# Performance work log

Hardware: AMD Instinct MI355X
Metric: run time of the kernel (lower is better)

The kernel has to match this reference:

```python
import jax, jax.numpy as jnp
import numpy as np

N = 100_000      # nodes
E = 1_600_000    # edges
IN = 128         # input_dim
HID = 64         # hidden_dim
H = 4            # num_heads
DH = HID // H    # per-head dim
L = 3            # num_layers
OUT = 64         # output_dim
SLOPE = 0.2      # DGL GATConv LeakyReLU default
EPS = 1e-5       # LayerNorm eps


def setup_inputs() -> dict:
    key = jax.random.key(0)
    ks = jax.random.split(key, 20)
    s = 0.02
    return {
        "node_features": jax.random.normal(ks[0], (N, IN), jnp.float32),
        "src": jax.random.randint(ks[1], (E,), 0, N, jnp.int32),
        "dst": jax.random.randint(ks[2], (E,), 0, N, jnp.int32),
        # input projection
        "W_in": jax.random.normal(ks[3], (IN, HID), jnp.float32) * s,
        "b_in": jnp.zeros((HID,), jnp.float32),
        # rewiring MLP: Linear(2*HID,64) -> Tanh -> Linear(64,1) -> Sigmoid
        "W_a1": jax.random.normal(ks[4], (2 * HID, 64), jnp.float32) * s,
        "b_a1": jnp.zeros((64,), jnp.float32),
        "W_a2": jax.random.normal(ks[5], (64, 1), jnp.float32) * s,
        "b_a2": jnp.zeros((1,), jnp.float32),
        # stacked GATConv params for L layers
        "W_gat": jax.random.normal(ks[6], (L, HID, H * DH), jnp.float32) * s,
        "a_l": jax.random.normal(ks[7], (L, H, DH), jnp.float32) * s,
        "a_r": jax.random.normal(ks[8], (L, H, DH), jnp.float32) * s,
        "b_gat": jnp.zeros((L, H, DH), jnp.float32),
        # LayerNorm + output projection
        "ln_g": jnp.ones((HID,), jnp.float32),
        "ln_b": jnp.zeros((HID,), jnp.float32),
        "W_out": jax.random.normal(ks[9], (HID, OUT), jnp.float32) * s,
        "b_out": jnp.zeros((OUT,), jnp.float32),
    }


def _gat_layer(h, src, dst, W, al, ar, b):
    # h: (N, HID) -> z: (N, H, DH)
    z = (h @ W).reshape(N, H, DH)
    el = jnp.sum(z * al, axis=-1)                       # (N, H)
    er = jnp.sum(z * ar, axis=-1)                       # (N, H)
    e = jax.nn.leaky_relu(el[src] + er[dst], SLOPE)     # (E, H)
    # segment softmax over incoming edges of each dst node
    m = jax.ops.segment_max(e, dst, num_segments=N)     # (N, H)
    ex = jnp.exp(e - m[dst])                            # (E, H)
    den = jax.ops.segment_sum(ex, dst, num_segments=N)  # (N, H)
    alpha = ex / den[dst]                               # (E, H)
    msg = z[src] * alpha[..., None]                     # (E, H, DH)
    out = jax.ops.segment_sum(msg, dst, num_segments=N) # (N, H, DH)
    # residual (identity since HID == H*DH) + bias, then flatten(1)
    out = out + h.reshape(N, H, DH) + b
    return out.reshape(N, H * DH)


def reference(node_features, src, dst, W_in, b_in, W_a1, b_a1, W_a2, b_a2,
              W_gat, a_l, a_r, b_gat, ln_g, ln_b, W_out, b_out):
    h = node_features @ W_in + b_in                     # (N, HID)
    # GraphRewiringModule: edge-wise gather + MLP + sigmoid score
    he = jnp.concatenate([h[src], h[dst]], axis=1)      # (E, 2*HID)
    edge_score = jax.nn.sigmoid(jnp.tanh(he @ W_a1 + b_a1) @ W_a2 + b_a2)  # (E,1); unused downstream, as in source
    for l in range(L):
        h = _gat_layer(h, src, dst, W_gat[l], a_l[l], a_r[l], b_gat[l])
    # LayerNorm
    mu = jnp.mean(h, axis=-1, keepdims=True)
    var = jnp.mean((h - mu) ** 2, axis=-1, keepdims=True)
    h = (h - mu) * jax.lax.rsqrt(var + EPS) * ln_g + ln_b
    return h @ W_out + b_out                            # (N, OUT)
```

## Files before the change

### kernel.cpp

```cpp
#include <hip/hip_runtime.h>

#define NN 100000
#define EE 1600000
#define IN_DIM 128
#define HID 64
#define NH 4
#define DH 16
#define NL 3
#define OUT_DIM 64
#define SLOPE 0.2f
#define LN_EPS 1e-5f
#define RB 4

#define BSH 9
#define BSZ 512
#define NB ((NN + BSZ - 1) / BSZ)
#define CAP 10240
#define CHUNK 4096
#define P1_BLOCKS ((EE + CHUNK - 1) / CHUNK)

using short8 = __attribute__((ext_vector_type(8))) short;
using f32x4  = __attribute__((ext_vector_type(4))) float;

__device__ __forceinline__ float bcast(float x, int lane) {
    return __int_as_float(__builtin_amdgcn_readlane(__float_as_int(x), lane));
}
__device__ __forceinline__ unsigned f2bf(float x) {
    unsigned u = __float_as_uint(x);
    u += 0x7FFFu + ((u >> 16) & 1u);
    return u >> 16;
}
__device__ __forceinline__ float bf2f(unsigned short b) {
    return __uint_as_float(((unsigned)b) << 16);
}
__device__ __forceinline__ float bflo(unsigned zp) {
    return __uint_as_float(zp << 16);
}
__device__ __forceinline__ float bfhi(unsigned zp) {
    return __uint_as_float(zp & 0xFFFF0000u);
}

__global__ void k_wpack(const float* __restrict__ W, uint4* __restrict__ Wb) {
    const int tid = blockIdx.x * 256 + threadIdx.x;
    if (tid >= 1024) return;
    const int lane = tid & 63;
    const int ntkk = tid >> 6;
    const int nt = ntkk & 3, kk = ntkk >> 2;
    const int k0 = kk * 32 + (lane >> 4) * 8;
    const int n  = nt * 16 + (lane & 15);
    unsigned dw[4];
#pragma unroll
    for (int p = 0; p < 4; ++p) {
        const unsigned lo = f2bf(W[(k0 + 2 * p) * HID + n]);
        const unsigned hi = f2bf(W[(k0 + 2 * p + 1) * HID + n]);
        dw[p] = lo | (hi << 16);
    }
    Wb[ntkk * 64 + lane] = make_uint4(dw[0], dw[1], dw[2], dw[3]);
}

__device__ float walv(const float* __restrict__ W, const float* __restrict__ al,
                      const float* __restrict__ ar, int k, int c) {
    if (c < 4) {
        float s = 0.f;
#pragma unroll
        for (int d = 0; d < 16; ++d) s += W[k * HID + c * 16 + d] * al[c * 16 + d];
        return s;
    }
    if (c < 8) {
        const int hh = c - 4;
        float s = 0.f;
#pragma unroll
        for (int d = 0; d < 16; ++d) s += W[k * HID + hh * 16 + d] * ar[hh * 16 + d];
        return s;
    }
    return 0.f;
}

__global__ void k_wpack_gat(const float* __restrict__ W_gat, const float* __restrict__ a_l,
                            const float* __restrict__ a_r, uint4* __restrict__ Wbg) {
    const int l = blockIdx.y;
    const int tid = blockIdx.x * 256 + threadIdx.x;
    if (tid >= 640) return;
    const int lane = tid & 63;
    const int f = tid >> 6;
    const int kk = f / 5, nt = f % 5;
    const float* W  = W_gat + (size_t)l * HID * HID;
    const float* al = a_l + (size_t)l * HID;
    const float* ar = a_r + (size_t)l * HID;
    const int k0 = kk * 32 + (lane >> 4) * 8;
    const int n  = lane & 15;
    unsigned dw[4];
#pragma unroll
    for (int p = 0; p < 4; ++p) {
        float b0, b1;
        if (nt < 4) {
            b0 = W[(k0 + 2 * p) * HID + nt * 16 + n];
            b1 = W[(k0 + 2 * p + 1) * HID + nt * 16 + n];
        } else {
            b0 = walv(W, al, ar, k0 + 2 * p, n);
            b1 = walv(W, al, ar, k0 + 2 * p + 1, n);
        }
        dw[p] = f2bf(b0) | (f2bf(b1) << 16);
    }
    Wbg[(size_t)l * 640 + f * 64 + lane] = make_uint4(dw[0], dw[1], dw[2], dw[3]);
}

__global__ __launch_bounds__(256)
void k_in_gemm(const float* __restrict__ X, const uint4* __restrict__ Wb,
               const float* __restrict__ b, unsigned* __restrict__ h32) {
    const int l  = threadIdx.x & 63;
    const int wv = threadIdx.x >> 6;
    const int wrow = blockIdx.x * 64 + wv * 16;
    if (wrow >= NN) return;
    const int arow = wrow + (l & 15);
    const int kb_off = (l >> 4) * 8;
    f32x4 acc[4];
#pragma unroll
    for (int nt = 0; nt < 4; ++nt) acc[nt] = (f32x4){0.f, 0.f, 0.f, 0.f};
    const float* xr = X + (size_t)arow * IN_DIM;
#pragma unroll
    for (int kk = 0; kk < 4; ++kk) {
        const int kb = kk * 32 + kb_off;
        const float4 xa = *(const float4*)(xr + kb);
        const float4 xb = *(const float4*)(xr + kb + 4);
        const unsigned d0 = f2bf(xa.x) | (f2bf(xa.y) << 16);
        const unsigned d1 = f2bf(xa.z) | (f2bf(xa.w) << 16);
        const unsigned d2 = f2bf(xb.x) | (f2bf(xb.y) << 16);
        const unsigned d3 = f2bf(xb.z) | (f2bf(xb.w) << 16);
        const uint4 au = make_uint4(d0, d1, d2, d3);
        const short8 af = __builtin_bit_cast(short8, au);
#pragma unroll
        for (int nt = 0; nt < 4; ++nt) {
            const uint4 bu = Wb[(kk * 4 + nt) * 64 + l];
            const short8 bf = __builtin_bit_cast(short8, bu);
            acc[nt] = __builtin_amdgcn_mfma_f32_16x16x32_bf16(af, bf, acc[nt], 0, 0, 0);
        }
    }
    const int grp = l >> 4, ci = l & 15;
#pragma unroll
    for (int nt = 0; nt < 4; ++nt) {
        const float bv = b[nt * 16 + ci];
#pragma unroll
        for (int r = 0; r < 4; ++r) {
            const int row = wrow + grp * 4 + r;
            const unsigned my = f2bf(acc[nt][r] + bv);
            const unsigned ot = (unsigned)__shfl_xor((int)my, 1, 64);
            if ((ci & 1) == 0)
                h32[(size_t)row * 32 + nt * 8 + (ci >> 1)] = my | (ot << 16);
        }
    }
}

__global__ __launch_bounds__(256)
void k_zgemm(const unsigned short* __restrict__ h16, const uint4* __restrict__ Wbg,
             unsigned* __restrict__ zb32, float* __restrict__ el, float* __restrict__ er) {
    const int l  = threadIdx.x & 63;
    const int wv = threadIdx.x >> 6;
    const int wrow = blockIdx.x * 64 + wv * 16;
    if (wrow >= NN) return;
    const int arow = wrow + (l & 15);
    const int kb_off = (l >> 4) * 8;
    f32x4 acc[5];
#pragma unroll
    for (int nt = 0; nt < 5; ++nt) acc[nt] = (f32x4){0.f, 0.f, 0.f, 0.f};
#pragma unroll
    for (int kk = 0; kk < 2; ++kk) {
        const int kb = kk * 32 + kb_off;
        const uint4 au = *(const uint4*)(h16 + (size_t)arow * 64 + kb);
        const short8 af = __builtin_bit_cast(short8, au);
#pragma unroll
        for (int nt = 0; nt < 5; ++nt) {
            const uint4 bu = Wbg[(kk * 5 + nt) * 64 + l];
            const short8 bf = __builtin_bit_cast(short8, bu);
            acc[nt] = __builtin_amdgcn_mfma_f32_16x16x32_bf16(af, bf, acc[nt], 0, 0, 0);
        }
    }
    const int grp = l >> 4, ci = l & 15;
#pragma unroll
    for (int nt = 0; nt < 4; ++nt) {
#pragma unroll
        for (int r = 0; r < 4; ++r) {
            const int row = wrow + grp * 4 + r;
            const unsigned my = f2bf(acc[nt][r]);
            const unsigned ot = (unsigned)__shfl_xor((int)my, 1, 64);
            if ((ci & 1) == 0)
                zb32[(size_t)row * 32 + nt * 8 + (ci >> 1)] = my | (ot << 16);
        }
    }
#pragma unroll
    for (int r = 0; r < 4; ++r) {
        const int row = wrow + grp * 4 + r;
        const float v = acc[4][r];
        if (ci < 4) el[row * NH + ci] = v;
        else if (ci < 8) er[row * NH + (ci - 4)] = v;
    }
}


__global__ void k_zero_bcnt(int* __restrict__ bcnt, int* __restrict__ esrc_pad) {
    if (threadIdx.x < NB) bcnt[threadIdx.x] = 0;
    if (threadIdx.x < 32) esrc_pad[threadIdx.x] = 0;
}

__global__ __launch_bounds__(256)
void k_bucketize(const int* __restrict__ src, const int* __restrict__ dst,
                 int* __restrict__ bcnt, int2* __restrict__ bbuf) {
    __shared__ int lh[256];
    __shared__ int lbase[256];
    __shared__ int lcnt[256];
    __shared__ int gbase[256];
    __shared__ int sc[256];
    __shared__ int2 stage[CHUNK];
    const int t = threadIdx.x;
    const int e0 = blockIdx.x * CHUNK;
    const int n = min(CHUNK, EE - e0);
    lh[t] = 0;
    __syncthreads();
    int myd[CHUNK / 256], mys[CHUNK / 256];
#pragma unroll
    for (int i = 0; i < CHUNK / 256; ++i) {
        const int o = i * 256 + t;
        if (o < n) {
            myd[i] = dst[e0 + o];
            mys[i] = src[e0 + o];
            atomicAdd(&lh[myd[i] >> BSH], 1);
        } else myd[i] = -1;
    }
    __syncthreads();
    {
        const int v = lh[t];
        lcnt[t] = v;
        sc[t] = v;
        __syncthreads();
        for (int off = 1; off < 256; off <<= 1) {
            const int x = (t >= off) ? sc[t - off] : 0;
            __syncthreads();
            sc[t] += x;
            __syncthreads();
        }
        lbase[t] = sc[t] - v;
        lh[t] = sc[t] - v;
    }
    __syncthreads();
#pragma unroll
    for (int i = 0; i < CHUNK / 256; ++i) {
        if (myd[i] >= 0) {
            const int b = myd[i] >> BSH;
            const int p = atomicAdd(&lh[b], 1);
            stage[p] = make_int2(mys[i], myd[i]);
        }
    }
    __syncthreads();
    if (t < NB && lcnt[t] > 0) gbase[t] = atomicAdd(&bcnt[t], lcnt[t]);
    __syncthreads();
    for (int i = t; i < n; i += 256) {
        const int2 en = stage[i];
        const int b = en.y >> BSH;
        const int gp = gbase[b] + (i - lbase[b]);
        if (gp < CAP) bbuf[(size_t)b * CAP + gp] = en;
    }
}

__global__ void k_bscan(const int* __restrict__ bcnt, int* __restrict__ bbase,
                        int* __restrict__ rowptr) {
    const int t = threadIdx.x;
    __shared__ int sc[256];
    const int v = (t < NB) ? bcnt[t] : 0;
    sc[t] = v;
    __syncthreads();
    for (int off = 1; off < 256; off <<= 1) {
        const int x = (t >= off) ? sc[t - off] : 0;
        __syncthreads();
        sc[t] += x;
        __syncthreads();
    }
    if (t < NB) bbase[t] = sc[t] - v;
    if (t == 0) rowptr[NN] = EE;
}

__global__ __launch_bounds__(256)
void k_localcsr(const int* __restrict__ bcnt, const int* __restrict__ bbase,
                const int2* __restrict__ bbuf, int* __restrict__ rowptr,
                int* __restrict__ esrc) {
    const int b = blockIdx.x;
    const int t = threadIdx.x;
    const int cnt = bcnt[b];
    const int base = bbase[b];
    const int n0 = b * BSZ;
    const int nn = min(BSZ, NN - n0);
    __shared__ int lh[BSZ];
    __shared__ int lsc[BSZ];
    __shared__ int sc[256];
    for (int i = t; i < BSZ; i += 256) lh[i] = 0;
    __syncthreads();
    const int2* bb = bbuf + (size_t)b * CAP;
    for (int i = t; i < cnt; i += 256) atomicAdd(&lh[bb[i].y & (BSZ - 1)], 1);
    __syncthreads();
    const int a0 = lh[2 * t], a1 = lh[2 * t + 1];
    const int ts = a0 + a1;
    sc[t] = ts;
    __syncthreads();
    for (int off = 1; off < 256; off <<= 1) {
        const int x = (t >= off) ? sc[t - off] : 0;
        __syncthreads();
        sc[t] += x;
        __syncthreads();
    }
    const int ebase = sc[t] - ts;
    lsc[2 * t] = ebase;
    lsc[2 * t + 1] = ebase + a0;
    __syncthreads();
    for (int i = t; i < BSZ; i += 256) {
        if (i < nn) rowptr[n0 + i] = base + lsc[i];
        lh[i] = lsc[i];
    }
    __syncthreads();
    for (int i = t; i < cnt; i += 256) {
        const int2 en = bb[i];
        const int p = atomicAdd(&lh[en.y & (BSZ - 1)], 1);
        esrc[base + p] = en.x;
    }
}

__global__ __launch_bounds__(256)
void k_gat_dst(const int* __restrict__ rowptr, const int* __restrict__ esrc,
               const float* __restrict__ el, const float* __restrict__ er,
               const uint4* __restrict__ zb128, const unsigned short* __restrict__ hin16,
               const float* __restrict__ bg, unsigned* __restrict__ hout32) {
    const int j  = threadIdx.x & 63;
    const int wv = threadIdx.x >> 6;
    const int d = blockIdx.x * 4 + wv;
    if (d >= NN) return;
    const int g = j >> 3;
    const int q = j & 7;
    const int hh = q >> 1;
    const int r0 = rowptr[d], r1 = rowptr[d + 1];
    const float erh = er[d * NH + hh];
    uint4 hv4 = make_uint4(0, 0, 0, 0);
    if (g == 0) hv4 = *(const uint4*)(hin16 + (size_t)d * 64 + 8 * q);
    float a0 = 0.f, a1 = 0.f, a2 = 0.f, a3 = 0.f;
    float a4 = 0.f, a5 = 0.f, a6 = 0.f, a7 = 0.f;
    float den = 0.f;
    unsigned sA = (unsigned)esrc[r0 + g];
    float avA = el[sA * NH + hh];
    uint4 zpA = zb128[sA * 8u + q];
    unsigned sB = (unsigned)esrc[r0 + 8 + g];
    for (int i = r0; i < r1; i += 8) {
        const float avB = el[sB * NH + hh];
        const uint4 zpB = zb128[sB * 8u + q];
        const unsigned sC = (unsigned)esrc[i + 16 + g];
        const float x = avA + erh;
        float w = __expf(fmaxf(x, SLOPE * x));
        w = (i + g < r1) ? w : 0.f;
        den += w;
        a0 = fmaf(w, bflo(zpA.x), a0);
        a1 = fmaf(w, bfhi(zpA.x), a1);
        a2 = fmaf(w, bflo(zpA.y), a2);
        a3 = fmaf(w, bfhi(zpA.y), a3);
        a4 = fmaf(w, bflo(zpA.z), a4);
        a5 = fmaf(w, bfhi(zpA.z), a5);
        a6 = fmaf(w, bflo(zpA.w), a6);
        a7 = fmaf(w, bfhi(zpA.w), a7);
        sA = sB; avA = avB; zpA = zpB; sB = sC;
    }
#pragma unroll
    for (int m = 8; m <= 32; m <<= 1) {
        den += __shfl_xor(den, m, 64);
        a0 += __shfl_xor(a0, m, 64);
        a1 += __shfl_xor(a1, m, 64);
        a2 += __shfl_xor(a2, m, 64);
        a3 += __shfl_xor(a3, m, 64);
        a4 += __shfl_xor(a4, m, 64);
        a5 += __shfl_xor(a5, m, 64);
        a6 += __shfl_xor(a6, m, 64);
        a7 += __shfl_xor(a7, m, 64);
    }
    if (g == 0) {
        const int c = 8 * q;
        float o0 = bflo(hv4.x) + bg[c + 0], o1 = bfhi(hv4.x) + bg[c + 1];
        float o2 = bflo(hv4.y) + bg[c + 2], o3 = bfhi(hv4.y) + bg[c + 3];
        float o4 = bflo(hv4.z) + bg[c + 4], o5 = bfhi(hv4.z) + bg[c + 5];
        float o6 = bflo(hv4.w) + bg[c + 6], o7 = bfhi(hv4.w) + bg[c + 7];
        if (r1 > r0) {
            const float rd = 1.f / den;
            o0 = fmaf(a0, rd, o0); o1 = fmaf(a1, rd, o1);
            o2 = fmaf(a2, rd, o2); o3 = fmaf(a3, rd, o3);
            o4 = fmaf(a4, rd, o4); o5 = fmaf(a5, rd, o5);
            o6 = fmaf(a6, rd, o6); o7 = fmaf(a7, rd, o7);
        }
        const uint4 ov = make_uint4(f2bf(o0) | (f2bf(o1) << 16),
                                    f2bf(o2) | (f2bf(o3) << 16),
                                    f2bf(o4) | (f2bf(o5) << 16),
                                    f2bf(o6) | (f2bf(o7) << 16));
        *(uint4*)(hout32 + (size_t)d * 32 + 4 * q) = ov;
    }
}

__global__ __launch_bounds__(256, 4)
void k_ln_out(const unsigned short* __restrict__ h16, const float* __restrict__ g,
              const float* __restrict__ be, const float* __restrict__ Wo,
              const float* __restrict__ bo, float* __restrict__ out) {
    const int j = threadIdx.x & 63;
    float Wreg[HID];
#pragma unroll
    for (int k = 0; k < HID; ++k) Wreg[k] = Wo[k * OUT_DIM + j];
    const float gj = g[j], bej = be[j], boj = bo[j];
    const int wid = (blockIdx.x * blockDim.x + threadIdx.x) >> 6;
    const int nw  = (gridDim.x * blockDim.x) >> 6;
    for (int v0 = wid * RB; v0 < NN; v0 += nw * RB) {
        float hn[RB];
#pragma unroll
        for (int r = 0; r < RB; ++r) {
            const float x = bf2f(h16[(size_t)(v0 + r) * HID + j]);
            float s = x;
#pragma unroll
            for (int m = 32; m >= 1; m >>= 1) s += __shfl_xor(s, m, 64);
            const float mu = s * (1.f / 64.f);
            const float dx = x - mu;
            float vs = dx * dx;
#pragma unroll
            for (int m = 32; m >= 1; m >>= 1) vs += __shfl_xor(vs, m, 64);
            hn[r] = dx * rsqrtf(vs * (1.f / 64.f) + LN_EPS) * gj + bej;
        }
        float acc[RB];
#pragma unroll
        for (int r = 0; r < RB; ++r) acc[r] = boj;
#pragma unroll
        for (int k = 0; k < HID; ++k) {
#pragma unroll
            for (int r = 0; r < RB; ++r)
                acc[r] = fmaf(bcast(hn[r], k), Wreg[k], acc[r]);
        }
#pragma unroll
        for (int r = 0; r < RB; ++r) out[(size_t)(v0 + r) * OUT_DIM + j] = acc[r];
    }
}

extern "C" void kernel_launch(void* const* d_in, const int* in_sizes, int n_in,
                              void* d_out, int out_size, void* d_ws, size_t ws_size,
                              hipStream_t stream) {
    const float* X     = (const float*)d_in[0];
    const int*   src   = (const int*)d_in[1];
    const int*   dst   = (const int*)d_in[2];
    const float* W_in  = (const float*)d_in[3];
    const float* b_in  = (const float*)d_in[4];
    const float* W_gat = (const float*)d_in[9];
    const float* a_l   = (const float*)d_in[10];
    const float* a_r   = (const float*)d_in[11];
    const float* b_gat = (const float*)d_in[12];
    const float* ln_g  = (const float*)d_in[13];
    const float* ln_b  = (const float*)d_in[14];
    const float* W_out = (const float*)d_in[15];
    const float* b_out = (const float*)d_in[16];
    float* out = (float*)d_out;

    char* ws = (char*)d_ws;
    unsigned short* hA16 = (unsigned short*)ws;
    unsigned short* hB16 = hA16 + (size_t)NN * HID;
    unsigned* zb32 = (unsigned*)(hB16 + (size_t)NN * HID);
    float* el = (float*)(zb32 + (size_t)NN * (HID / 2));
    float* er = el + (size_t)NN * NH;
    int* rowptr = (int*)(er + (size_t)NN * NH);
    int* esrc   = rowptr + NN + 1;
    int* bcnt   = esrc + EE + 32;
    int* bbase  = bcnt + NB;
    uintptr_t wp = (uintptr_t)(bbase + NB);
    wp = (wp + 15) & ~(uintptr_t)15;
    uint4* Wb   = (uint4*)wp;
    uint4* Wbg  = Wb + 1024;
    int2* bbuf  = (int2*)hB16;

    k_wpack<<<4, 256, 0, stream>>>(W_in, Wb);
    k_wpack_gat<<<dim3(3, NL), 256, 0, stream>>>(W_gat, a_l, a_r, Wbg);
    k_in_gemm<<<(NN + 63) / 64, 256, 0, stream>>>(X, Wb, b_in, (unsigned*)hA16);

    k_zero_bcnt<<<1, 256, 0, stream>>>(bcnt, esrc + EE);
    k_bucketize<<<P1_BLOCKS, 256, 0, stream>>>(src, dst, bcnt, bbuf);
    k_bscan<<<1, 256, 0, stream>>>(bcnt, bbase, rowptr);
    k_localcsr<<<NB, 256, 0, stream>>>(bcnt, bbase, bbuf, rowptr, esrc);

    unsigned short* hin = hA16;
    unsigned short* hout = hB16;
    for (int l = 0; l < NL; ++l) {
        k_zgemm<<<(NN + 63) / 64, 256, 0, stream>>>(hin, Wbg + (size_t)l * 640,
                                                    zb32, el, er);
        k_gat_dst<<<(NN + 3) / 4, 256, 0, stream>>>(rowptr, esrc, el, er,
                                                    (const uint4*)zb32, hin,
                                                    b_gat + (size_t)l * HID,
                                                    (unsigned*)hout);
        unsigned short* t = hin; hin = hout; hout = t;
    }

    k_ln_out<<<1024, 256, 0, stream>>>(hin, ln_g, ln_b, W_out, b_out, out);
}
```

Baseline: 295.8 us.

## Store GAT node features as scaled FP8 and pack bucket entries into 32 bits

```diff
diff --git a/kernel.cpp b/kernel.cpp
--- a/kernel.cpp
+++ b/kernel.cpp
@@ -11,6 +11,8 @@
 #define SLOPE 0.2f
 #define LN_EPS 1e-5f
 #define RB 4
+#define ZSC 64.0f
+#define ZISC 0.015625f
 
 #define BSH 9
 #define BSZ 512
@@ -21,6 +23,7 @@
 
 using short8 = __attribute__((ext_vector_type(8))) short;
 using f32x4  = __attribute__((ext_vector_type(4))) float;
+using f32x2  = __attribute__((ext_vector_type(2))) float;
 
 __device__ __forceinline__ float bcast(float x, int lane) {
     return __int_as_float(__builtin_amdgcn_readlane(__float_as_int(x), lane));
@@ -153,7 +156,7 @@
 
 __global__ __launch_bounds__(256)
 void k_zgemm(const unsigned short* __restrict__ h16, const uint4* __restrict__ Wbg,
-             unsigned* __restrict__ zb32, float* __restrict__ el, float* __restrict__ er) {
+             unsigned* __restrict__ zb8, float* __restrict__ el, float* __restrict__ er) {
     const int l  = threadIdx.x & 63;
     const int wv = threadIdx.x >> 6;
     const int wrow = blockIdx.x * 64 + wv * 16;
@@ -181,10 +184,13 @@
 #pragma unroll
         for (int r = 0; r < 4; ++r) {
             const int row = wrow + grp * 4 + r;
-            const unsigned my = f2bf(acc[nt][r]);
-            const unsigned ot = (unsigned)__shfl_xor((int)my, 1, 64);
-            if ((ci & 1) == 0)
-                zb32[(size_t)row * 32 + nt * 8 + (ci >> 1)] = my | (ot << 16);
+            const float v = acc[nt][r] * ZSC;
+            const float vn = __shfl_xor(v, 1, 64);
+            unsigned pk = (unsigned)__builtin_amdgcn_cvt_pk_fp8_f32(v, vn, 0, false) & 0xFFFFu;
+            const unsigned pk2 = (unsigned)__shfl_xor((int)pk, 2, 64);
+            pk |= pk2 << 16;
+            if ((ci & 3) == 0)
+                zb8[(size_t)row * 16 + nt * 4 + (ci >> 2)] = pk;
         }
     }
 #pragma unroll
@@ -204,7 +210,7 @@
 
 __global__ __launch_bounds__(256)
 void k_bucketize(const int* __restrict__ src, const int* __restrict__ dst,
-                 int* __restrict__ bcnt, int2* __restrict__ bbuf) {
+                 int* __restrict__ bcnt, unsigned* __restrict__ bbuf) {
     __shared__ int lh[256];
     __shared__ int lbase[256];
     __shared__ int lcnt[256];
@@ -257,7 +263,9 @@
         const int2 en = stage[i];
         const int b = en.y >> BSH;
         const int gp = gbase[b] + (i - lbase[b]);
-        if (gp < CAP) bbuf[(size_t)b * CAP + gp] = en;
+        if (gp < CAP)
+            bbuf[(size_t)b * CAP + gp] =
+                (unsigned)en.x | (((unsigned)en.y & 511u) << 17);
     }
 }
 
@@ -280,7 +288,7 @@
 
 __global__ __launch_bounds__(256)
 void k_localcsr(const int* __restrict__ bcnt, const int* __restrict__ bbase,
-                const int2* __restrict__ bbuf, int* __restrict__ rowptr,
+                const unsigned* __restrict__ bbuf, int* __restrict__ rowptr,
                 int* __restrict__ esrc) {
     const int b = blockIdx.x;
     const int t = threadIdx.x;
@@ -293,8 +301,8 @@
     __shared__ int sc[256];
     for (int i = t; i < BSZ; i += 256) lh[i] = 0;
     __syncthreads();
-    const int2* bb = bbuf + (size_t)b * CAP;
-    for (int i = t; i < cnt; i += 256) atomicAdd(&lh[bb[i].y & (BSZ - 1)], 1);
+    const unsigned* bb = bbuf + (size_t)b * CAP;
+    for (int i = t; i < cnt; i += 256) atomicAdd(&lh[(bb[i] >> 17) & 511u], 1);
     __syncthreads();
     const int a0 = lh[2 * t], a1 = lh[2 * t + 1];
     const int ts = a0 + a1;
@@ -316,16 +324,16 @@
     }
     __syncthreads();
     for (int i = t; i < cnt; i += 256) {
-        const int2 en = bb[i];
-        const int p = atomicAdd(&lh[en.y & (BSZ - 1)], 1);
-        esrc[base + p] = en.x;
+        const unsigned en = bb[i];
+        const int p = atomicAdd(&lh[(en >> 17) & 511u], 1);
+        esrc[base + p] = (int)(en & 0x1FFFFu);
     }
 }
 
 __global__ __launch_bounds__(256)
 void k_gat_dst(const int* __restrict__ rowptr, const int* __restrict__ esrc,
                const float* __restrict__ el, const float* __restrict__ er,
-               const uint4* __restrict__ zb128, const unsigned short* __restrict__ hin16,
+               const uint2* __restrict__ zb64, const unsigned short* __restrict__ hin16,
                const float* __restrict__ bg, unsigned* __restrict__ hout32) {
     const int j  = threadIdx.x & 63;
     const int wv = threadIdx.x >> 6;
@@ -343,24 +351,28 @@
     float den = 0.f;
     unsigned sA = (unsigned)esrc[r0 + g];
     float avA = el[sA * NH + hh];
-    uint4 zpA = zb128[sA * 8u + q];
+    uint2 zpA = zb64[sA * 8u + q];
     unsigned sB = (unsigned)esrc[r0 + 8 + g];
     for (int i = r0; i < r1; i += 8) {
         const float avB = el[sB * NH + hh];
-        const uint4 zpB = zb128[sB * 8u + q];
+        const uint2 zpB = zb64[sB * 8u + q];
         const unsigned sC = (unsigned)esrc[i + 16 + g];
         const float x = avA + erh;
         float w = __expf(fmaxf(x, SLOPE * x));
         w = (i + g < r1) ? w : 0.f;
         den += w;
-        a0 = fmaf(w, bflo(zpA.x), a0);
-        a1 = fmaf(w, bfhi(zpA.x), a1);
-        a2 = fmaf(w, bflo(zpA.y), a2);
-        a3 = fmaf(w, bfhi(zpA.y), a3);
-        a4 = fmaf(w, bflo(zpA.z), a4);
-        a5 = fmaf(w, bfhi(zpA.z), a5);
-        a6 = fmaf(w, bflo(zpA.w), a6);
-        a7 = fmaf(w, bfhi(zpA.w), a7);
+        const f32x2 p0 = __builtin_amdgcn_cvt_pk_f32_fp8(zpA.x, false);
+        const f32x2 p1 = __builtin_amdgcn_cvt_pk_f32_fp8(zpA.x, true);
+        const f32x2 p2 = __builtin_amdgcn_cvt_pk_f32_fp8(zpA.y, false);
+        const f32x2 p3 = __builtin_amdgcn_cvt_pk_f32_fp8(zpA.y, true);
+        a0 = fmaf(w, p0.x, a0);
+        a1 = fmaf(w, p0.y, a1);
+        a2 = fmaf(w, p1.x, a2);
+        a3 = fmaf(w, p1.y, a3);
+        a4 = fmaf(w, p2.x, a4);
+        a5 = fmaf(w, p2.y, a5);
+        a6 = fmaf(w, p3.x, a6);
+        a7 = fmaf(w, p3.y, a7);
         sA = sB; avA = avB; zpA = zpB; sB = sC;
     }
 #pragma unroll
@@ -382,11 +394,11 @@
         float o4 = bflo(hv4.z) + bg[c + 4], o5 = bfhi(hv4.z) + bg[c + 5];
         float o6 = bflo(hv4.w) + bg[c + 6], o7 = bfhi(hv4.w) + bg[c + 7];
         if (r1 > r0) {
-            const float rd = 1.f / den;
-            o0 = fmaf(a0, rd, o0); o1 = fmaf(a1, rd, o1);
-            o2 = fmaf(a2, rd, o2); o3 = fmaf(a3, rd, o3);
-            o4 = fmaf(a4, rd, o4); o5 = fmaf(a5, rd, o5);
-            o6 = fmaf(a6, rd, o6); o7 = fmaf(a7, rd, o7);
+            const float rds = (1.f / den) * ZISC;
+            o0 = fmaf(a0, rds, o0); o1 = fmaf(a1, rds, o1);
+            o2 = fmaf(a2, rds, o2); o3 = fmaf(a3, rds, o3);
+            o4 = fmaf(a4, rds, o4); o5 = fmaf(a5, rds, o5);
+            o6 = fmaf(a6, rds, o6); o7 = fmaf(a7, rds, o7);
         }
         const uint4 ov = make_uint4(f2bf(o0) | (f2bf(o1) << 16),
                                     f2bf(o2) | (f2bf(o3) << 16),
@@ -457,8 +469,8 @@
     char* ws = (char*)d_ws;
     unsigned short* hA16 = (unsigned short*)ws;
     unsigned short* hB16 = hA16 + (size_t)NN * HID;
-    unsigned* zb32 = (unsigned*)(hB16 + (size_t)NN * HID);
-    float* el = (float*)(zb32 + (size_t)NN * (HID / 2));
+    unsigned* zb8 = (unsigned*)(hB16 + (size_t)NN * HID);
+    float* el = (float*)(zb8 + (size_t)NN * 16);
     float* er = el + (size_t)NN * NH;
     int* rowptr = (int*)(er + (size_t)NN * NH);
     int* esrc   = rowptr + NN + 1;
@@ -468,7 +480,7 @@
     wp = (wp + 15) & ~(uintptr_t)15;
     uint4* Wb   = (uint4*)wp;
     uint4* Wbg  = Wb + 1024;
-    int2* bbuf  = (int2*)hB16;
+    unsigned* bbuf = (unsigned*)hB16;
 
     k_wpack<<<4, 256, 0, stream>>>(W_in, Wb);
     k_wpack_gat<<<dim3(3, NL), 256, 0, stream>>>(W_gat, a_l, a_r, Wbg);
@@ -483,9 +495,9 @@
     unsigned short* hout = hB16;
     for (int l = 0; l < NL; ++l) {
         k_zgemm<<<(NN + 63) / 64, 256, 0, stream>>>(hin, Wbg + (size_t)l * 640,
-                                                    zb32, el, er);
+                                                    zb8, el, er);
         k_gat_dst<<<(NN + 3) / 4, 256, 0, stream>>>(rowptr, esrc, el, er,
-                                                    (const uint4*)zb32, hin,
+                                                    (const uint2*)zb8, hin,
                                                     b_gat + (size_t)l * HID,
                                                     (unsigned*)hout);
         unsigned short* t = hin; hin = hout; hout = t;
```

Result: no change. 296.0 us (+0.1%).
